# Kernel optimization log

Hardware: AMD Instinct MI355X
Metric: run time of the kernel (lower is better)

Reference implementation:

```python
import jax, jax.numpy as jnp
import numpy as np

N_EMBD = 1024
N_HEAD = 16
D_HEAD = N_EMBD // N_HEAD


def setup_inputs() -> dict:
    key = jax.random.key(0)
    ks = jax.random.split(key, 5)
    x = jax.random.normal(ks[0], (4, 2048, N_EMBD), dtype=jnp.float32)
    s = 1.0 / np.sqrt(N_EMBD)
    Wq = jax.random.normal(ks[1], (N_EMBD, N_EMBD), dtype=jnp.float32) * s
    Wk = jax.random.normal(ks[2], (N_EMBD, N_EMBD), dtype=jnp.float32) * s
    Wv = jax.random.normal(ks[3], (N_EMBD, N_EMBD), dtype=jnp.float32) * s
    Wo = jax.random.normal(ks[4], (N_EMBD, N_EMBD), dtype=jnp.float32) * s
    return {"x": x, "Wq": Wq, "Wk": Wk, "Wv": Wv, "Wo": Wo}


def reference(x, Wq, Wk, Wv, Wo):
    B, S, E = x.shape
    H, Dh = N_HEAD, D_HEAD
    scale = 1.0 / np.sqrt(Dh)  # LayerwiseSDPA(d_head) -> scale by 1/sqrt(d_head)

    def proj(W):
        # nn.Linear(no bias): y = x @ W.T ; reshape to [B,H,S,Dh]
        return (x @ W.T).reshape(B, S, H, Dh).transpose(0, 2, 1, 3)

    q, k, v = proj(Wq), proj(Wk), proj(Wv)
    scores = jnp.einsum('bhsd,bhtd->bhst', q, k) * scale  # [B,H,S,S]
    causal = jnp.tril(jnp.ones((S, S), dtype=bool))
    scores = jnp.where(causal, scores, jnp.finfo(scores.dtype).min)
    attn = jax.nn.softmax(scores, axis=-1)
    y = jnp.einsum('bhst,bhtd->bhsd', attn, v)  # [B,H,S,Dh]
    y = y.transpose(0, 2, 1, 3).reshape(B, S, E)
    return y @ Wo.T
```

## Files before the change

kernel.cpp:

```cpp
#include <hip/hip_runtime.h>

typedef __bf16 bf16;
typedef bf16  bf16x8 __attribute__((ext_vector_type(8)));
typedef bf16  bf16x4 __attribute__((ext_vector_type(4)));
typedef short s16x4  __attribute__((ext_vector_type(4)));
typedef float f32x4  __attribute__((ext_vector_type(4)));

#define AS1 __attribute__((address_space(1)))
#define AS3 __attribute__((address_space(3)))

#define SQLEN 2048
#define EMB   1024

__global__ __launch_bounds__(256) void cvt_f32_bf16(const float* __restrict__ in,
                                                    bf16* __restrict__ out, int n8) {
  int i = blockIdx.x * blockDim.x + threadIdx.x;
  if (i >= n8) return;
  const float4* p = (const float4*)in + (size_t)i * 2;
  float4 a = p[0], b = p[1];
  bf16x8 o;
  o[0] = (bf16)a.x; o[1] = (bf16)a.y; o[2] = (bf16)a.z; o[3] = (bf16)a.w;
  o[4] = (bf16)b.x; o[5] = (bf16)b.y; o[6] = (bf16)b.z; o[7] = (bf16)b.w;
  *((bf16x8*)out + i) = o;
}

__global__ __launch_bounds__(256) void cvt_w4(const float* __restrict__ w0, const float* __restrict__ w1,
                                              const float* __restrict__ w2, const float* __restrict__ w3,
                                              bf16* o0, bf16* o1, bf16* o2, bf16* o3, int n8) {
  const float* in; bf16* out;
  switch (blockIdx.y) {
    case 0: in = w0; out = o0; break;
    case 1: in = w1; out = o1; break;
    case 2: in = w2; out = o2; break;
    default: in = w3; out = o3; break;
  }
  int i = blockIdx.x * blockDim.x + threadIdx.x;
  if (i >= n8) return;
  const float4* p = (const float4*)in + (size_t)i * 2;
  float4 a = p[0], b = p[1];
  bf16x8 o;
  o[0] = (bf16)a.x; o[1] = (bf16)a.y; o[2] = (bf16)a.z; o[3] = (bf16)a.w;
  o[4] = (bf16)b.x; o[5] = (bf16)b.y; o[6] = (bf16)b.z; o[7] = (bf16)b.w;
  *((bf16x8*)out + i) = o;
}

__device__ __forceinline__
void gemm_body_f32(const bf16* __restrict__ A, const bf16* __restrict__ B,
                   float* __restrict__ Cf, int M, int N, int K,
                   bf16* Asl, bf16* Bsl) {
  const int tid  = threadIdx.x;
  const int lane = tid & 63, wave = tid >> 6;
  const int quad = lane >> 4, col = lane & 15;
  const int m0 = blockIdx.x * 128, n0 = blockIdx.y * 128;
  const int wr = wave >> 1, wc = wave & 1;

  f32x4 acc[4][4];
  const f32x4 fz = {0.f, 0.f, 0.f, 0.f};
#pragma unroll
  for (int i = 0; i < 4; ++i)
#pragma unroll
    for (int j = 0; j < 4; ++j) acc[i][j] = fz;

  const int srow = lane >> 2;
  const int sk   = lane & 3;

  auto stage = [&](int buf, int k0) {
#pragma unroll
    for (int r = 0; r < 2; ++r) {
      const int c      = wave * 2 + r;
      const int row    = c * 16 + srow;
      const int gchunk = sk ^ (row & 3);
      const bf16* ga = A + (size_t)(m0 + row) * K + k0 + gchunk * 8;
      const bf16* gb = B + (size_t)(n0 + row) * K + k0 + gchunk * 8;
      __builtin_amdgcn_global_load_lds((const AS1 void*)ga, (AS3 void*)(Asl + buf * 4096 + c * 512), 16, 0, 0);
      __builtin_amdgcn_global_load_lds((const AS1 void*)gb, (AS3 void*)(Bsl + buf * 4096 + c * 512), 16, 0, 0);
    }
  };

  const int nk = K >> 5;
  stage(0, 0);
  for (int it = 0; it < nk; ++it) {
    __syncthreads();
    if (it + 1 < nk) stage((it + 1) & 1, (it + 1) << 5);
    const bf16* As = Asl + (it & 1) * 4096;
    const bf16* Bs = Bsl + (it & 1) * 4096;

    bf16x8 af[4], bfr[4];
#pragma unroll
    for (int i = 0; i < 4; ++i) {
      const int r = wr * 64 + i * 16 + col;
      af[i] = *(const bf16x8*)&As[r * 32 + ((quad ^ (col & 3)) * 8)];
    }
#pragma unroll
    for (int j = 0; j < 4; ++j) {
      const int r = wc * 64 + j * 16 + col;
      bfr[j] = *(const bf16x8*)&Bs[r * 32 + ((quad ^ (col & 3)) * 8)];
    }
#pragma unroll
    for (int i = 0; i < 4; ++i)
#pragma unroll
      for (int j = 0; j < 4; ++j)
        acc[i][j] = __builtin_amdgcn_mfma_f32_16x16x32_bf16(af[i], bfr[j], acc[i][j], 0, 0, 0);
  }

#pragma unroll
  for (int i = 0; i < 4; ++i) {
#pragma unroll
    for (int j = 0; j < 4; ++j) {
      const int gm0 = m0 + wr * 64 + i * 16 + quad * 4;
      const int gn  = n0 + wc * 64 + j * 16 + col;
#pragma unroll
      for (int r = 0; r < 4; ++r)
        Cf[(size_t)(gm0 + r) * N + gn] = acc[i][j][r];
    }
  }
}

__global__ __launch_bounds__(256, 2)
void gemm_qkv(const bf16* __restrict__ A, const bf16* __restrict__ Wq,
              const bf16* __restrict__ Wk, const bf16* __restrict__ Wv,
              bf16* __restrict__ Qo, bf16* __restrict__ Ko, bf16* __restrict__ Vto,
              float qscale) {
  __shared__ bf16 Asl[2 * 4096];
  __shared__ bf16 Bsl[3][2 * 4096];

  const int tid  = threadIdx.x;
  const int lane = tid & 63, wave = tid >> 6;
  const int quad = lane >> 4, col = lane & 15;
  const int m0 = blockIdx.x * 128, n0 = blockIdx.y * 128;
  const int wr = wave >> 1, wc = wave & 1;
  const int K = 1024, N = 1024;

  const bf16* const Bp[3] = {Wq, Wk, Wv};

  f32x4 acc[3][4][4];
  const f32x4 fz = {0.f, 0.f, 0.f, 0.f};
#pragma unroll
  for (int s = 0; s < 3; ++s)
#pragma unroll
    for (int i = 0; i < 4; ++i)
#pragma unroll
      for (int j = 0; j < 4; ++j) acc[s][i][j] = fz;

  const int srow = lane >> 2;
  const int sk   = lane & 3;

  auto stage = [&](int buf, int k0) {
#pragma unroll
    for (int r = 0; r < 2; ++r) {
      const int c      = wave * 2 + r;
      const int row    = c * 16 + srow;
      const int gchunk = sk ^ (row & 3);
      const bf16* ga = A + (size_t)(m0 + row) * K + k0 + gchunk * 8;
      __builtin_amdgcn_global_load_lds((const AS1 void*)ga,
          (AS3 void*)(Asl + buf * 4096 + c * 512), 16, 0, 0);
#pragma unroll
      for (int s = 0; s < 3; ++s) {
        const bf16* gb = Bp[s] + (size_t)(n0 + row) * K + k0 + gchunk * 8;
        __builtin_amdgcn_global_load_lds((const AS1 void*)gb,
            (AS3 void*)(&Bsl[s][buf * 4096 + c * 512]), 16, 0, 0);
      }
    }
  };

  const int nk = K >> 5;
  stage(0, 0);
  for (int it = 0; it < nk; ++it) {
    __syncthreads();
    if (it + 1 < nk) stage((it + 1) & 1, (it + 1) << 5);
    const bf16* As = Asl + (it & 1) * 4096;

    bf16x8 af[4];
#pragma unroll
    for (int i = 0; i < 4; ++i) {
      const int r = wr * 64 + i * 16 + col;
      af[i] = *(const bf16x8*)&As[r * 32 + ((quad ^ (col & 3)) * 8)];
    }
#pragma unroll
    for (int s = 0; s < 3; ++s) {
      const bf16* Bs = &Bsl[s][(it & 1) * 4096];
      bf16x8 bfr[4];
#pragma unroll
      for (int j = 0; j < 4; ++j) {
        const int r = wc * 64 + j * 16 + col;
        bfr[j] = *(const bf16x8*)&Bs[r * 32 + ((quad ^ (col & 3)) * 8)];
      }
#pragma unroll
      for (int i = 0; i < 4; ++i)
#pragma unroll
        for (int j = 0; j < 4; ++j)
          acc[s][i][j] = __builtin_amdgcn_mfma_f32_16x16x32_bf16(af[i], bfr[j], acc[s][i][j], 0, 0, 0);
    }
  }

#pragma unroll
  for (int s = 0; s < 3; ++s) {
    const float sc = (s == 0) ? qscale : 1.0f;
#pragma unroll
    for (int i = 0; i < 4; ++i) {
#pragma unroll
      for (int j = 0; j < 4; ++j) {
        const int gm0 = m0 + wr * 64 + i * 16 + quad * 4;
        const int gn  = n0 + wc * 64 + j * 16 + col;
        if (s == 2) {
          bf16x4 ob;
#pragma unroll
          for (int r = 0; r < 4; ++r) ob[r] = (bf16)(acc[s][i][j][r]);
          const int bb = gm0 >> 11;
          const int t_ = gm0 & 2047;
          *(bf16x4*)&Vto[((size_t)(bb * 1024 + gn)) * 2048 + t_] = ob;
        } else {
          bf16* C = (s == 0) ? Qo : Ko;
#pragma unroll
          for (int r = 0; r < 4; ++r)
            C[(size_t)(gm0 + r) * N + gn] = (bf16)(acc[s][i][j][r] * sc);
        }
      }
    }
  }
}

__global__ __launch_bounds__(256, 2)
void gemm_o(const bf16* __restrict__ A, const bf16* __restrict__ W, float* __restrict__ C) {
  __shared__ bf16 Asl[2 * 4096];
  __shared__ bf16 Bsl[2 * 4096];
  gemm_body_f32(A, W, C, 8192, 1024, 1024, Asl, Bsl);
}

__global__ __launch_bounds__(256, 2)
void attn_flash(const bf16* __restrict__ Q, const bf16* __restrict__ K,
                const bf16* __restrict__ Vt, bf16* __restrict__ Y) {
  __shared__ bf16 Ksb0[2 * 8192];
  __shared__ bf16 Vsb0[2 * 8192];

  const int tid  = threadIdx.x;
  const int lane = tid & 63, wave = tid >> 6;
  const int quad = lane >> 4, col = lane & 15;

  const int B_ = blockIdx.x;
  const int bh = (B_ & 7) * 8 + (B_ >> 6);
  const int p  = (B_ >> 3) & 7;
  const int h  = bh & 15;
  const int b  = bh >> 4;
  const int hc = h * 64;
  const size_t rowBase = (size_t)b * SQLEN;

  const int srow8 = lane >> 3;
  const int sch   = lane & 7;
  const int a7    = col & 7;

  auto stageKV = [&](int buf, int t0) {
#pragma unroll
    for (int i = 0; i < 4; ++i) {
      const int krow = wave * 32 + i * 8 + srow8;
      const int kch  = sch ^ srow8;
      const bf16* gk = K + (rowBase + t0 + krow) * EMB + hc + kch * 8;
      __builtin_amdgcn_global_load_lds((const AS1 void*)gk,
          (AS3 void*)(Ksb0 + buf * 8192 + wave * 2048 + i * 512), 16, 0, 0);
      const int vrow = wave * 16 + i * 4 + (lane >> 4);
      const int vch  = (lane & 15) ^ (vrow & 7);
      const bf16* gv = Vt + ((size_t)(b * EMB + hc + vrow)) * SQLEN + t0 + vch * 8;
      __builtin_amdgcn_global_load_lds((const AS1 void*)gv,
          (AS3 void*)(Vsb0 + buf * 8192 + wave * 2048 + i * 512), 16, 0, 0);
    }
  };

  const s16x4 ones = {(short)0x3F80, (short)0x3F80, (short)0x3F80, (short)0x3F80};

  for (int halfIdx = 0; halfIdx < 2; ++halfIdx) {
    const int qt = halfIdx == 0 ? (15 - p) : p;
    const int q0 = qt * 128;
    const int ntt = qt + 1;

    stageKV(0, 0);

    bf16x8 qf[2][2];
#pragma unroll
    for (int g = 0; g < 2; ++g) {
      const int row = g * 64 + wave * 16 + col;
      const bf16* gq = Q + (rowBase + q0 + row) * EMB + hc + quad * 8;
      qf[g][0] = *(const bf16x8*)gq;
      qf[g][1] = *(const bf16x8*)(gq + 32);
    }
    __syncthreads();

    float m_i[2] = {-INFINITY, -INFINITY};
    f32x4 o[2][4], ol[2];
    const f32x4 fz = {0.f, 0.f, 0.f, 0.f};
#pragma unroll
    for (int g = 0; g < 2; ++g) {
#pragma unroll
      for (int dd = 0; dd < 4; ++dd) o[g][dd] = fz;
      ol[g] = fz;
    }

    for (int tt = 0; tt < ntt; ++tt) {
      const int t0 = tt * 128;
      const int cur = tt & 1;
      if (tt + 1 < ntt) stageKV(cur ^ 1, t0 + 128);
      const bf16* Ks = Ksb0 + cur * 8192;
      const bf16* Vs = Vsb0 + cur * 8192;

      f32x4 s[2][8];
      __builtin_amdgcn_s_setprio(1);
#pragma unroll
      for (int sl = 0; sl < 8; ++sl) {
        const bf16x8 kf0 = *(const bf16x8*)&Ks[(sl * 16 + col) * 64 + ((quad ^ a7) * 8)];
        const bf16x8 kf1 = *(const bf16x8*)&Ks[(sl * 16 + col) * 64 + (((quad ^ 4) ^ a7) * 8)];
#pragma unroll
        for (int g = 0; g < 2; ++g) {
          f32x4 z = fz;
          z = __builtin_amdgcn_mfma_f32_16x16x32_bf16(kf0, qf[g][0], z, 0, 0, 0);
          s[g][sl] = __builtin_amdgcn_mfma_f32_16x16x32_bf16(kf1, qf[g][1], z, 0, 0, 0);
        }
      }
      __builtin_amdgcn_s_setprio(0);

      if (tt == qt) {
#pragma unroll
        for (int g = 0; g < 2; ++g) {
          const int qg = q0 + g * 64 + wave * 16 + col;
#pragma unroll
          for (int sl = 0; sl < 8; ++sl)
#pragma unroll
            for (int r = 0; r < 4; ++r)
              if (t0 + sl * 16 + quad * 4 + r > qg) s[g][sl][r] = -INFINITY;
        }
      }

      bf16x4 pb[2][8];
#pragma unroll
      for (int g = 0; g < 2; ++g) {
        float mx = s[g][0][0];
#pragma unroll
        for (int sl = 0; sl < 8; ++sl)
#pragma unroll
          for (int r = 0; r < 4; ++r) mx = fmaxf(mx, s[g][sl][r]);
        mx = fmaxf(mx, __shfl_xor(mx, 16));
        mx = fmaxf(mx, __shfl_xor(mx, 32));
        if (!__all(mx <= m_i[g] + 8.f)) {
          const float mnew = fmaxf(m_i[g], mx);
          const float a = __builtin_amdgcn_exp2f(m_i[g] - mnew);
#pragma unroll
          for (int dd = 0; dd < 4; ++dd) o[g][dd] *= a;
          ol[g] *= a;
          m_i[g] = mnew;
        }
#pragma unroll
        for (int sl = 0; sl < 8; ++sl)
#pragma unroll
          for (int r = 0; r < 4; ++r)
            pb[g][sl][r] = (bf16)__builtin_amdgcn_exp2f(s[g][sl][r] - m_i[g]);
      }

      __builtin_amdgcn_s_setprio(1);
#pragma unroll
      for (int sl = 0; sl < 8; ++sl) {
        const s16x4 pf0 = __builtin_bit_cast(s16x4, pb[0][sl]);
        const s16x4 pf1 = __builtin_bit_cast(s16x4, pb[1][sl]);
        ol[0] = __builtin_amdgcn_mfma_f32_16x16x16bf16_1k(ones, pf0, ol[0], 0, 0, 0);
        ol[1] = __builtin_amdgcn_mfma_f32_16x16x16bf16_1k(ones, pf1, ol[1], 0, 0, 0);
        const int cch  = 2 * sl + (quad >> 1);
        const int half = quad & 1;
#pragma unroll
        for (int dd = 0; dd < 4; ++dd) {
          const int row = dd * 16 + col;
          const bf16x4 vb = *(const bf16x4*)&Vs[row * 128 + ((cch ^ a7) * 8) + half * 4];
          const s16x4 vf = __builtin_bit_cast(s16x4, vb);
          o[0][dd] = __builtin_amdgcn_mfma_f32_16x16x16bf16_1k(vf, pf0, o[0][dd], 0, 0, 0);
          o[1][dd] = __builtin_amdgcn_mfma_f32_16x16x16bf16_1k(vf, pf1, o[1][dd], 0, 0, 0);
        }
      }
      __builtin_amdgcn_s_setprio(0);
      __syncthreads();
    }

#pragma unroll
    for (int g = 0; g < 2; ++g) {
      const float rl = __builtin_amdgcn_rcpf(ol[g][0]);
      const size_t yrow = (rowBase + q0 + g * 64 + wave * 16 + col) * EMB + hc;
#pragma unroll
      for (int dd = 0; dd < 4; ++dd) {
        bf16x4 ob;
#pragma unroll
        for (int r = 0; r < 4; ++r) ob[r] = (bf16)(o[g][dd][r] * rl);
        *(bf16x4*)&Y[yrow + dd * 16 + quad * 4] = ob;
      }
    }
  }
}

extern "C" void kernel_launch(void* const* d_in, const int* in_sizes, int n_in,
                              void* d_out, int out_size, void* d_ws, size_t ws_size,
                              hipStream_t stream) {
  const float* x  = (const float*)d_in[0];
  const float* Wq = (const float*)d_in[1];
  const float* Wk = (const float*)d_in[2];
  const float* Wv = (const float*)d_in[3];
  const float* Wo = (const float*)d_in[4];
  float* out = (float*)d_out;

  const size_t ME = 8192ull * 1024ull;
  const size_t WE = 1024ull * 1024ull;
  bf16* ws  = (bf16*)d_ws;
  bf16* xb  = ws;
  bf16* wqb = xb + ME;
  bf16* wkb = wqb + WE;
  bf16* wvb = wkb + WE;
  bf16* wob = wvb + WE;
  bf16* Qb  = wob + WE;
  bf16* Kb  = Qb + ME;
  bf16* Vtb = Kb + ME;
  bf16* Yb  = Vtb + ME;

  cvt_f32_bf16<<<(int)(ME / 8 / 256), 256, 0, stream>>>(x, xb, (int)(ME / 8));
  cvt_w4<<<dim3((int)(WE / 8 / 256), 4), 256, 0, stream>>>(Wq, Wk, Wv, Wo, wqb, wkb, wvb, wob, (int)(WE / 8));

  const float qscale = 0.125f * 1.4426950408889634f;
  gemm_qkv<<<dim3(64, 8), 256, 0, stream>>>(xb, wqb, wkb, wvb, Qb, Kb, Vtb, qscale);

  attn_flash<<<512, 256, 0, stream>>>(Qb, Kb, Vtb, Yb);

  gemm_o<<<dim3(64, 8), 256, 0, stream>>>(Yb, wob, out);
}
```

Measured before the change: 243.3 us.

## Interleave per-group QK, softmax and PV phases to overlap MFMA with exp

```diff
diff --git a/kernel.cpp b/kernel.cpp
--- a/kernel.cpp
+++ b/kernel.cpp
@@ -266,6 +266,7 @@
   };
 
   const s16x4 ones = {(short)0x3F80, (short)0x3F80, (short)0x3F80, (short)0x3F80};
+  const f32x4 fz = {0.f, 0.f, 0.f, 0.f};
 
   for (int halfIdx = 0; halfIdx < 2; ++halfIdx) {
     const int qt = halfIdx == 0 ? (15 - p) : p;
@@ -286,7 +287,6 @@
 
     float m_i[2] = {-INFINITY, -INFINITY};
     f32x4 o[2][4], ol[2];
-    const f32x4 fz = {0.f, 0.f, 0.f, 0.f};
 #pragma unroll
     for (int g = 0; g < 2; ++g) {
 #pragma unroll
@@ -301,65 +301,70 @@
       const bf16* Ks = Ksb0 + cur * 8192;
       const bf16* Vs = Vsb0 + cur * 8192;
 
-      f32x4 s[2][8];
-      __builtin_amdgcn_s_setprio(1);
+      f32x4 s0[8];
 #pragma unroll
       for (int sl = 0; sl < 8; ++sl) {
         const bf16x8 kf0 = *(const bf16x8*)&Ks[(sl * 16 + col) * 64 + ((quad ^ a7) * 8)];
         const bf16x8 kf1 = *(const bf16x8*)&Ks[(sl * 16 + col) * 64 + (((quad ^ 4) ^ a7) * 8)];
-#pragma unroll
-        for (int g = 0; g < 2; ++g) {
-          f32x4 z = fz;
-          z = __builtin_amdgcn_mfma_f32_16x16x32_bf16(kf0, qf[g][0], z, 0, 0, 0);
-          s[g][sl] = __builtin_amdgcn_mfma_f32_16x16x32_bf16(kf1, qf[g][1], z, 0, 0, 0);
-        }
-      }
-      __builtin_amdgcn_s_setprio(0);
-
+        f32x4 z = fz;
+        z = __builtin_amdgcn_mfma_f32_16x16x32_bf16(kf0, qf[0][0], z, 0, 0, 0);
+        s0[sl] = __builtin_amdgcn_mfma_f32_16x16x32_bf16(kf1, qf[0][1], z, 0, 0, 0);
+      }
       if (tt == qt) {
-#pragma unroll
-        for (int g = 0; g < 2; ++g) {
-          const int qg = q0 + g * 64 + wave * 16 + col;
-#pragma unroll
-          for (int sl = 0; sl < 8; ++sl)
-#pragma unroll
-            for (int r = 0; r < 4; ++r)
-              if (t0 + sl * 16 + quad * 4 + r > qg) s[g][sl][r] = -INFINITY;
-        }
-      }
-
-      bf16x4 pb[2][8];
-#pragma unroll
-      for (int g = 0; g < 2; ++g) {
-        float mx = s[g][0][0];
-#pragma unroll
-        for (int sl = 0; sl < 8; ++sl)
-#pragma unroll
-          for (int r = 0; r < 4; ++r) mx = fmaxf(mx, s[g][sl][r]);
+        const int qg = q0 + wave * 16 + col;
+#pragma unroll
+        for (int sl = 0; sl < 8; ++sl)
+#pragma unroll
+          for (int r = 0; r < 4; ++r)
+            if (t0 + sl * 16 + quad * 4 + r > qg) s0[sl][r] = -INFINITY;
+      }
+
+      bf16x4 pb0[8];
+      {
+        float mx = s0[0][0];
+#pragma unroll
+        for (int sl = 0; sl < 8; ++sl)
+#pragma unroll
+          for (int r = 0; r < 4; ++r) mx = fmaxf(mx, s0[sl][r]);
         mx = fmaxf(mx, __shfl_xor(mx, 16));
         mx = fmaxf(mx, __shfl_xor(mx, 32));
-        if (!__all(mx <= m_i[g] + 8.f)) {
-          const float mnew = fmaxf(m_i[g], mx);
-          const float a = __builtin_amdgcn_exp2f(m_i[g] - mnew);
-#pragma unroll
-          for (int dd = 0; dd < 4; ++dd) o[g][dd] *= a;
-          ol[g] *= a;
-          m_i[g] = mnew;
+        if (!__all(mx <= m_i[0] + 8.f)) {
+          const float mnew = fmaxf(m_i[0], mx);
+          const float a = __builtin_amdgcn_exp2f(m_i[0] - mnew);
+#pragma unroll
+          for (int dd = 0; dd < 4; ++dd) o[0][dd] *= a;
+          ol[0] *= a;
+          m_i[0] = mnew;
         }
 #pragma unroll
         for (int sl = 0; sl < 8; ++sl)
 #pragma unroll
           for (int r = 0; r < 4; ++r)
-            pb[g][sl][r] = (bf16)__builtin_amdgcn_exp2f(s[g][sl][r] - m_i[g]);
-      }
-
-      __builtin_amdgcn_s_setprio(1);
+            pb0[sl][r] = (bf16)__builtin_amdgcn_exp2f(s0[sl][r] - m_i[0]);
+      }
+
+      f32x4 s1[8];
 #pragma unroll
       for (int sl = 0; sl < 8; ++sl) {
-        const s16x4 pf0 = __builtin_bit_cast(s16x4, pb[0][sl]);
-        const s16x4 pf1 = __builtin_bit_cast(s16x4, pb[1][sl]);
+        const bf16x8 kf0 = *(const bf16x8*)&Ks[(sl * 16 + col) * 64 + ((quad ^ a7) * 8)];
+        const bf16x8 kf1 = *(const bf16x8*)&Ks[(sl * 16 + col) * 64 + (((quad ^ 4) ^ a7) * 8)];
+        f32x4 z = fz;
+        z = __builtin_amdgcn_mfma_f32_16x16x32_bf16(kf0, qf[1][0], z, 0, 0, 0);
+        s1[sl] = __builtin_amdgcn_mfma_f32_16x16x32_bf16(kf1, qf[1][1], z, 0, 0, 0);
+      }
+      if (tt == qt) {
+        const int qg = q0 + 64 + wave * 16 + col;
+#pragma unroll
+        for (int sl = 0; sl < 8; ++sl)
+#pragma unroll
+          for (int r = 0; r < 4; ++r)
+            if (t0 + sl * 16 + quad * 4 + r > qg) s1[sl][r] = -INFINITY;
+      }
+
+#pragma unroll
+      for (int sl = 0; sl < 8; ++sl) {
+        const s16x4 pf0 = __builtin_bit_cast(s16x4, pb0[sl]);
         ol[0] = __builtin_amdgcn_mfma_f32_16x16x16bf16_1k(ones, pf0, ol[0], 0, 0, 0);
-        ol[1] = __builtin_amdgcn_mfma_f32_16x16x16bf16_1k(ones, pf1, ol[1], 0, 0, 0);
         const int cch  = 2 * sl + (quad >> 1);
         const int half = quad & 1;
 #pragma unroll
@@ -368,10 +373,48 @@
           const bf16x4 vb = *(const bf16x4*)&Vs[row * 128 + ((cch ^ a7) * 8) + half * 4];
           const s16x4 vf = __builtin_bit_cast(s16x4, vb);
           o[0][dd] = __builtin_amdgcn_mfma_f32_16x16x16bf16_1k(vf, pf0, o[0][dd], 0, 0, 0);
+        }
+      }
+
+      bf16x4 pb1[8];
+      {
+        float mx = s1[0][0];
+#pragma unroll
+        for (int sl = 0; sl < 8; ++sl)
+#pragma unroll
+          for (int r = 0; r < 4; ++r) mx = fmaxf(mx, s1[sl][r]);
+        mx = fmaxf(mx, __shfl_xor(mx, 16));
+        mx = fmaxf(mx, __shfl_xor(mx, 32));
+        if (!__all(mx <= m_i[1] + 8.f)) {
+          const float mnew = fmaxf(m_i[1], mx);
+          const float a = __builtin_amdgcn_exp2f(m_i[1] - mnew);
+#pragma unroll
+          for (int dd = 0; dd < 4; ++dd) o[1][dd] *= a;
+          ol[1] *= a;
+          m_i[1] = mnew;
+        }
+#pragma unroll
+        for (int sl = 0; sl < 8; ++sl)
+#pragma unroll
+          for (int r = 0; r < 4; ++r)
+            pb1[sl][r] = (bf16)__builtin_amdgcn_exp2f(s1[sl][r] - m_i[1]);
+      }
+
+#pragma unroll
+      for (int sl = 0; sl < 8; ++sl) {
+        const s16x4 pf1 = __builtin_bit_cast(s16x4, pb1[sl]);
+        ol[1] = __builtin_amdgcn_mfma_f32_16x16x16bf16_1k(ones, pf1, ol[1], 0, 0, 0);
+        const int cch  = 2 * sl + (quad >> 1);
+        const int half = quad & 1;
+#pragma unroll
+        for (int dd = 0; dd < 4; ++dd) {
+          const int row = dd * 16 + col;
+          const bf16x4 vb = *(const bf16x4*)&Vs[row * 128 + ((cch ^ a7) * 8) + half * 4];
+          const s16x4 vf = __builtin_bit_cast(s16x4, vb);
           o[1][dd] = __builtin_amdgcn_mfma_f32_16x16x16bf16_1k(vf, pf1, o[1][dd], 0, 0, 0);
         }
       }
-      __builtin_amdgcn_s_setprio(0);
+
       __syncthreads();
     }
 
```

Result: no change. 246.1 us (+1.2%).
